# Kernel tuning notes

Measured on AMD Instinct MI355X. Metric: run time of the kernel, lower is better.

The kernel has to match this reference:

```python
import jax, jax.numpy as jnp
import numpy as np

D_MODEL = 64
N_HEADS = 4
HEAD_DIM = D_MODEL // N_HEADS
D_FF = 128
EPS = 1e-5


def _layernorm(x, gamma, beta):
    mu = jnp.mean(x, axis=-1, keepdims=True)
    var = jnp.mean(jnp.square(x - mu), axis=-1, keepdims=True)
    return (x - mu) * jax.lax.rsqrt(var + EPS) * gamma + beta


def setup_inputs() -> dict:
    key = jax.random.key(0)
    ks = jax.random.split(key, 8)
    b, t = 16, 2048
    s = 0.05  # weight init scale
    return {
        "x": jax.random.normal(ks[0], (b, t, D_MODEL), dtype=jnp.float32),
        "Wqkv": jax.random.normal(ks[1], (3 * D_MODEL, D_MODEL), dtype=jnp.float32) * s,
        "Wproj": jax.random.normal(ks[2], (D_MODEL, D_MODEL), dtype=jnp.float32) * s,
        "W1": jax.random.normal(ks[3], (D_FF, D_MODEL), dtype=jnp.float32) * s,
        "b1": jax.random.normal(ks[4], (D_FF,), dtype=jnp.float32) * s,
        "W2": jax.random.normal(ks[5], (D_MODEL, D_FF), dtype=jnp.float32) * s,
        "b2": jax.random.normal(ks[6], (D_MODEL,), dtype=jnp.float32) * s,
        "g1": jnp.ones((D_MODEL,), dtype=jnp.float32),
        "be1": jnp.zeros((D_MODEL,), dtype=jnp.float32),
        "g2": jnp.ones((D_MODEL,), dtype=jnp.float32),
        "be2": jnp.zeros((D_MODEL,), dtype=jnp.float32),
    }


def reference(x, Wqkv, Wproj, W1, b1, W2, b2, g1, be1, g2, be2):
    b, t, c = x.shape
    # qkv: [b,t,3c] -> [b,t,3,h,hd] -> unbind into q,k,v each [b,h,t,hd]
    qkv = jnp.einsum('btc,ec->bte', x, Wqkv)
    qkv = qkv.reshape(b, t, 3, N_HEADS, HEAD_DIM)
    q = jnp.transpose(qkv[:, :, 0], (0, 2, 1, 3))
    k = jnp.transpose(qkv[:, :, 1], (0, 2, 1, 3))
    v = jnp.transpose(qkv[:, :, 2], (0, 2, 1, 3))
    scale = HEAD_DIM ** -0.5
    attn = jnp.einsum('bhqd,bhkd->bhqk', q, k) * scale  # [b,h,t,t]
    attn = jax.nn.softmax(attn, axis=-1)
    a = jnp.einsum('bhqk,bhkd->bhqd', attn, v)          # [b,h,t,hd]
    a = jnp.transpose(a, (0, 2, 1, 3)).reshape(b, t, c)
    a = jnp.einsum('btc,dc->btd', a, Wproj)
    x = _layernorm(x + a, g1, be1)
    y = jnp.einsum('btc,fc->btf', x, W1) + b1
    y = jnp.einsum('btf,cf->btc', jax.nn.relu(y), W2) + b2
    return _layernorm(x + y, g2, be2)
```

## Files before the change

kernel.cpp:

```cpp
#include <hip/hip_runtime.h>
#include <hip/hip_bf16.h>
#include <math.h>

typedef _Float16 h16;
typedef h16   v4h __attribute__((ext_vector_type(4)));
typedef h16   h2  __attribute__((ext_vector_type(2)));
typedef float v4f __attribute__((ext_vector_type(4)));

#define T_SEQ 2048
#define BATCH 16
#define NTOK  (BATCH * T_SEQ)
#define C_DIM 64
#define N_H   4
#define HD    16
#define FF    128
#define EPS_LN 1e-5f
#define MFMA16 __builtin_amdgcn_mfma_f32_16x16x16f16
#define QSCALE (0.25f * 1.44269504089f * 1024.0f)
#define BMAGIC (12582912.0f + 15316.0f)

static __device__ __forceinline__ float frcp(float x) {
#if __has_builtin(__builtin_amdgcn_rcpf)
    return __builtin_amdgcn_rcpf(x);
#else
    return 1.0f / x;
#endif
}
static __device__ __forceinline__ float frsq(float x) {
#if __has_builtin(__builtin_amdgcn_rsqf)
    return __builtin_amdgcn_rsqf(x);
#else
    return rsqrtf(x);
#endif
}
static __device__ __forceinline__ float fdot2p(h2 a, float acc) {
#if __has_builtin(__builtin_amdgcn_fdot2)
    const h2 one2 = {(h16)1.0f, (h16)1.0f};
    return __builtin_amdgcn_fdot2(a, one2, acc, false);
#else
    return acc + (float)a[0] + (float)a[1];
#endif
}
static __device__ __forceinline__ v4h cvt4(v4f f) {
    v4h r; r[0]=(h16)f[0]; r[1]=(h16)f[1]; r[2]=(h16)f[2]; r[3]=(h16)f[3];
    return r;
}
static __device__ __forceinline__ h2 pkperm(float t0, float t1) {
    unsigned r = __builtin_amdgcn_perm(__builtin_bit_cast(unsigned, t1),
                                       __builtin_bit_cast(unsigned, t0),
                                       0x05040100u);
    return __builtin_bit_cast(h2, r);
}

__global__ __launch_bounds__(256) void prep_pack(
    const float* __restrict__ Wqkv, const float* __restrict__ Wproj,
    const float* __restrict__ W1,   const float* __restrict__ W2,
    v4h* __restrict__ wp)
{
    int fid = blockIdx.x * 256 + threadIdx.x;
    int lane = fid & 63;
    int lm = lane & 15, g4 = ((lane >> 4) & 3) * 4;
    int frag = fid >> 6;
    const float* src; int o, kt, K;
    if (fid < 3072)      { int f = frag;      o = f >> 2; kt = f & 3; K = 64;  src = Wqkv;  }
    else if (fid < 4096) { int f = frag - 48; o = f >> 2; kt = f & 3; K = 64;  src = Wproj; }
    else if (fid < 6144) { int f = frag - 64; o = f >> 2; kt = f & 3; K = 64;  src = W1;    }
    else                 { int f = frag - 96; o = f >> 3; kt = f & 7; K = 128; src = W2;    }
    v4f v = *(const v4f*)(src + (o*16 + lm)*K + kt*16 + g4);
    wp[fid] = cvt4(v);
}

__global__ __launch_bounds__(256) void qkv_gemm(
    const float* __restrict__ x, const v4h* __restrict__ wq,
    h16* __restrict__ q, h16* __restrict__ k, h16* __restrict__ vt)
{
    int tid = threadIdx.x;
    int lane = tid & 63, w = tid >> 6;
    int lm = lane & 15, g4 = (lane >> 4) * 4;
    int gw = blockIdx.x * 4 + w;
    int tile = gw >> 2, ng = gw & 3;
    int t0 = tile * 16;

    v4h af[4];
#pragma unroll
    for (int kt = 0; kt < 4; kt++)
        af[kt] = cvt4(*(const v4f*)(x + (size_t)(t0 + lm) * C_DIM + kt * 16 + g4));

    int b = t0 >> 11, tl = t0 & (T_SEQ - 1);
#pragma unroll
    for (int j = 0; j < 3; j++) {
        int n = ng * 3 + j;
        v4f acc = {0.f, 0.f, 0.f, 0.f};
#pragma unroll
        for (int kt = 0; kt < 4; kt++)
            acc = MFMA16(af[kt], wq[(n*4 + kt)*64 + lane], acc, 0, 0, 0);
        if (n < 4) {
            h16* qp = q + ((size_t)(b*N_H + n)*T_SEQ + tl + g4)*HD + lm;
#pragma unroll
            for (int r = 0; r < 4; r++) qp[r*HD] = (h16)(acc[r] * QSCALE);
        } else if (n < 8) {
            h16* kp = k + ((size_t)(b*N_H + (n-4))*T_SEQ + tl + g4)*HD + lm;
#pragma unroll
            for (int r = 0; r < 4; r++) kp[r*HD] = (h16)acc[r];
        } else {
            v4h pk;
#pragma unroll
            for (int r = 0; r < 4; r++) pk[r] = (h16)acc[r];
            *(v4h*)(vt + ((size_t)(b*N_H + (n-8))*(T_SEQ/16) + (tl >> 4))*256
                       + lm*16 + g4) = pk;
        }
    }
}

__global__ __launch_bounds__(256, 8) void attn_mfma(
    const h16* __restrict__ q, const h16* __restrict__ k,
    const h16* __restrict__ vt, h16* __restrict__ a)
{
    int tid = threadIdx.x;
    int lane = tid & 63, w = tid >> 6;
    int lm = lane & 15, g4 = (lane >> 4) * 4;
    int bid = blockIdx.x;
    int W = (bid & 7) * 256 + (bid >> 3);
    int bh = W >> 5;
    int q64 = W & 31;
    int q0 = q64 * 64 + (w & 1) * 32;
    int khalf = w >> 1;

    v4h qf0 = *(const v4h*)(q + ((size_t)bh*T_SEQ + q0      + lm)*HD + g4);
    v4h qf1 = *(const v4h*)(q + ((size_t)bh*T_SEQ + q0 + 16 + lm)*HD + g4);
    const h16* kpl = k  + ((size_t)bh*T_SEQ + khalf*1024 + lm)*HD + g4;
    const h16* vpl = vt + ((size_t)bh*(T_SEQ/16) + khalf*64)*256 + lm*16 + g4;

    v4f accA0={0,0,0,0}, accB0={0,0,0,0}, accA1={0,0,0,0}, accB1={0,0,0,0};
    float l0a = 0.f, l0b = 0.f, l1a = 0.f, l1b = 0.f;
    const v4f bvec = {BMAGIC, BMAGIC, BMAGIC, BMAGIC};

    for (int kt = 0; kt < 16; kt++) {
        v4h kf[4], vf[4];
#pragma unroll
        for (int m = 0; m < 4; m++) {
            kf[m] = *(const v4h*)(kpl + m*256);
            vf[m] = *(const v4h*)(vpl + m*256);
        }
        kpl += 1024; vpl += 1024;
        __builtin_amdgcn_sched_barrier(0);
#pragma unroll
        for (int m = 0; m < 4; m++) {
            v4f t0v = MFMA16(kf[m], qf0, bvec, 0, 0, 0);
            v4f t1v = MFMA16(kf[m], qf1, bvec, 0, 0, 0);
            h2 a0 = pkperm(t0v[0], t0v[1]);
            h2 b0 = pkperm(t0v[2], t0v[3]);
            h2 a1 = pkperm(t1v[0], t1v[1]);
            h2 b1 = pkperm(t1v[2], t1v[3]);
            l0a = fdot2p(a0, l0a); l0b = fdot2p(b0, l0b);
            l1a = fdot2p(a1, l1a); l1b = fdot2p(b1, l1b);
            v4h p0 = __builtin_shufflevector(a0, b0, 0, 1, 2, 3);
            v4h p1 = __builtin_shufflevector(a1, b1, 0, 1, 2, 3);
            if (m & 1) { accB0 = MFMA16(vf[m], p0, accB0, 0,0,0); accB1 = MFMA16(vf[m], p1, accB1, 0,0,0); }
            else       { accA0 = MFMA16(vf[m], p0, accA0, 0,0,0); accA1 = MFMA16(vf[m], p1, accA1, 0,0,0); }
        }
    }

    float l0 = l0a + l0b, l1 = l1a + l1b;
    l0 += __shfl_xor(l0, 16, 64); l0 += __shfl_xor(l0, 32, 64);
    l1 += __shfl_xor(l1, 16, 64); l1 += __shfl_xor(l1, 32, 64);
    v4f acc0 = accA0 + accB0, acc1 = accA1 + accB1;

    __shared__ float lds[2][64][13];
    if (w >= 2) {
        float* p = lds[w - 2][lane];
        p[0] = l0; p[1] = l1;
#pragma unroll
        for (int r = 0; r < 4; r++) { p[2 + r] = acc0[r]; p[6 + r] = acc1[r]; }
    }
    __syncthreads();
    if (w < 2) {
        const float* p = lds[w][lane];
        float inv0 = frcp(l0 + p[0]);
        float inv1 = frcp(l1 + p[1]);
        int b = bh >> 2, h = bh & 3;
        v4h o0, o1;
#pragma unroll
        for (int r = 0; r < 4; r++) {
            o0[r] = (h16)((acc0[r] + p[2 + r]) * inv0);
            o1[r] = (h16)((acc1[r] + p[6 + r]) * inv1);
        }
        *(v4h*)(a + ((size_t)(b*T_SEQ) + q0      + lm)*C_DIM + h*HD + g4) = o0;
        *(v4h*)(a + ((size_t)(b*T_SEQ) + q0 + 16 + lm)*C_DIM + h*HD + g4) = o1;
    }
}

__global__ __launch_bounds__(256) void tail_fused(
    const h16* __restrict__ a, const float* __restrict__ x,
    const v4h* __restrict__ wp,
    const float* __restrict__ b1, const float* __restrict__ b2,
    const float* __restrict__ g1, const float* __restrict__ be1,
    const float* __restrict__ g2, const float* __restrict__ be2,
    float* __restrict__ out)
{
    int tid = threadIdx.x;
    int lane = tid & 63, w = tid >> 6;
    int lm = lane & 15, g4 = (lane >> 4) * 4;
    int pair = w >> 1;
    int half = w & 1;
    int t0 = (blockIdx.x * 2 + pair) * 16;

    const v4h* whp = wp + 3072;
    const v4h* wh1 = wp + 4096;
    const v4h* wh2 = wp + 6144;

    v4h af[4];
#pragma unroll
    for (int kt = 0; kt < 4; kt++)
        af[kt] = *(const v4h*)(a + (size_t)(t0 + lm)*C_DIM + kt*16 + g4);

    float rvn[4][4];
    v4h x1t[4];
    {
        v4h wf[16];
#pragma unroll
        for (int f = 0; f < 16; f++) wf[f] = whp[f*64 + lane];
        __builtin_amdgcn_sched_barrier(0);
        v4f rv[4];
#pragma unroll
        for (int cn = 0; cn < 4; cn++) {
            v4f acc = {0.f, 0.f, 0.f, 0.f};
#pragma unroll
            for (int kt = 0; kt < 4; kt++)
                acc = MFMA16(wf[cn*4 + kt], af[kt], acc, 0, 0, 0);
            v4f xr = *(const v4f*)(x + (size_t)(t0 + lm)*C_DIM + cn*16 + g4);
            rv[cn] = acc + xr;
        }
        float s = 0.f;
#pragma unroll
        for (int cn = 0; cn < 4; cn++)
#pragma unroll
            for (int i = 0; i < 4; i++) s += rv[cn][i];
        s += __shfl_xor(s, 16, 64); s += __shfl_xor(s, 32, 64);
        float mu = s * (1.f/64.f);
        float qs = 0.f;
#pragma unroll
        for (int cn = 0; cn < 4; cn++)
#pragma unroll
            for (int i = 0; i < 4; i++) { float d = rv[cn][i] - mu; qs += d*d; }
        qs += __shfl_xor(qs, 16, 64); qs += __shfl_xor(qs, 32, 64);
        float is = frsq(qs * (1.f/64.f) + EPS_LN);
#pragma unroll
        for (int cn = 0; cn < 4; cn++) {
            v4f g1v = *(const v4f*)(g1 + cn*16 + g4);
            v4f bev = *(const v4f*)(be1 + cn*16 + g4);
#pragma unroll
            for (int i = 0; i < 4; i++) {
                float vl = (rv[cn][i] - mu) * is * g1v[i] + bev[i];
                rvn[cn][i] = vl;
                x1t[cn][i] = (h16)vl;
            }
        }
    }
    __builtin_amdgcn_sched_barrier(0);

    v4h ht[4];
    {
        v4h wf[16];
#pragma unroll
        for (int f = 0; f < 16; f++) wf[f] = wh1[(half*16 + f)*64 + lane];
        __builtin_amdgcn_sched_barrier(0);
#pragma unroll
        for (int j = 0; j < 4; j++) {
            int nf = half * 4 + j;
            v4f acc = {0.f, 0.f, 0.f, 0.f};
#pragma unroll
            for (int kt = 0; kt < 4; kt++)
                acc = MFMA16(wf[j*4 + kt], x1t[kt], acc, 0, 0, 0);
            v4f b1v = *(const v4f*)(b1 + nf*16 + g4);
#pragma unroll
            for (int i = 0; i < 4; i++) ht[j][i] = (h16)fmaxf(acc[i] + b1v[i], 0.f);
        }
    }
    __builtin_amdgcn_sched_barrier(0);

    float yp[4][4];
    {
        v4h wf[16];
#pragma unroll
        for (int cn = 0; cn < 4; cn++)
#pragma unroll
            for (int j = 0; j < 4; j++)
                wf[cn*4 + j] = wh2[(cn*8 + half*4 + j)*64 + lane];
        __builtin_amdgcn_sched_barrier(0);
#pragma unroll
        for (int cn = 0; cn < 4; cn++) {
            v4f acc = {0.f, 0.f, 0.f, 0.f};
#pragma unroll
            for (int j = 0; j < 4; j++)
                acc = MFMA16(wf[cn*4 + j], ht[j], acc, 0, 0, 0);
#pragma unroll
            for (int i = 0; i < 4; i++) yp[cn][i] = acc[i];
        }
    }

    __shared__ float lds[2][64][17];
    if (half == 1) {
        float* p = lds[pair][lane];
#pragma unroll
        for (int cn = 0; cn < 4; cn++)
#pragma unroll
            for (int i = 0; i < 4; i++) p[cn*4 + i] = yp[cn][i];
    }
    __syncthreads();
    if (half == 0) {
        const float* p = lds[pair][lane];
        float yv[4][4];
#pragma unroll
        for (int cn = 0; cn < 4; cn++) {
            v4f b2v = *(const v4f*)(b2 + cn*16 + g4);
#pragma unroll
            for (int i = 0; i < 4; i++)
                yv[cn][i] = yp[cn][i] + p[cn*4 + i] + b2v[i] + rvn[cn][i];
        }
        float s2 = 0.f;
#pragma unroll
        for (int cn = 0; cn < 4; cn++)
#pragma unroll
            for (int i = 0; i < 4; i++) s2 += yv[cn][i];
        s2 += __shfl_xor(s2, 16, 64); s2 += __shfl_xor(s2, 32, 64);
        float mu2 = s2 * (1.f/64.f);
        float qs2 = 0.f;
#pragma unroll
        for (int cn = 0; cn < 4; cn++)
#pragma unroll
            for (int i = 0; i < 4; i++) { float d = yv[cn][i] - mu2; qs2 += d*d; }
        qs2 += __shfl_xor(qs2, 16, 64); qs2 += __shfl_xor(qs2, 32, 64);
        float is2 = frsq(qs2 * (1.f/64.f) + EPS_LN);
#pragma unroll
        for (int cn = 0; cn < 4; cn++) {
            v4f g2v = *(const v4f*)(g2 + cn*16 + g4);
            v4f bev = *(const v4f*)(be2 + cn*16 + g4);
            v4f o;
#pragma unroll
            for (int i = 0; i < 4; i++) o[i] = (yv[cn][i] - mu2) * is2 * g2v[i] + bev[i];
            *(v4f*)(out + (size_t)(t0 + lm)*C_DIM + cn*16 + g4) = o;
        }
    }
}

extern "C" void kernel_launch(void* const* d_in, const int* in_sizes, int n_in,
                              void* d_out, int out_size, void* d_ws, size_t ws_size,
                              hipStream_t stream)
{
    const float* x     = (const float*)d_in[0];
    const float* Wqkv  = (const float*)d_in[1];
    const float* Wproj = (const float*)d_in[2];
    const float* W1    = (const float*)d_in[3];
    const float* b1    = (const float*)d_in[4];
    const float* W2    = (const float*)d_in[5];
    const float* b2    = (const float*)d_in[6];
    const float* g1    = (const float*)d_in[7];
    const float* be1   = (const float*)d_in[8];
    const float* g2    = (const float*)d_in[9];
    const float* be2   = (const float*)d_in[10];
    float* out = (float*)d_out;

    const size_t perQ = (size_t)BATCH * N_H * T_SEQ * HD;
    h16* q   = (h16*)d_ws;
    h16* kk  = q  + perQ;
    h16* vt  = kk + perQ;
    h16* a   = vt + perQ;
    v4h* wp  = (v4h*)(a + (size_t)NTOK * C_DIM);

    prep_pack  <<<32,   256, 0, stream>>>(Wqkv, Wproj, W1, W2, wp);
    qkv_gemm   <<<2048, 256, 0, stream>>>(x, wp, q, kk, vt);
    attn_mfma  <<<2048, 256, 0, stream>>>(q, kk, vt, a);
    tail_fused <<<1024, 256, 0, stream>>>(a, x, wp, b1, b2,
                                          g1, be1, g2, be2, out);
}
```

Baseline: 69.99 us.

## Switch to 16x16x32 f16 MFMA with repacked weights and V layout

Replaces pairs of 16x16x16 MFMAs with the K=32 variant available on MI355X (gfx950) across the QKV GEMM, attention PV product, and tail GEMMs. It repacks the weight fragments and the transposed V buffer into 8-half fragments so each lane loads one 16-byte vector per MFMA. The goal is to halve the MFMA issue count and widen the loads. The PV accumulation now waits for all four score tiles before issuing, which reduces interleaving between the softmax work and the MFMAs.

```diff
diff --git a/kernel.cpp b/kernel.cpp
--- a/kernel.cpp
+++ b/kernel.cpp
@@ -4,6 +4,7 @@
 
 typedef _Float16 h16;
 typedef h16   v4h __attribute__((ext_vector_type(4)));
+typedef h16   v8h __attribute__((ext_vector_type(8)));
 typedef h16   h2  __attribute__((ext_vector_type(2)));
 typedef float v4f __attribute__((ext_vector_type(4)));
 
@@ -16,6 +17,7 @@
 #define FF    128
 #define EPS_LN 1e-5f
 #define MFMA16 __builtin_amdgcn_mfma_f32_16x16x16f16
+#define MFMA32K __builtin_amdgcn_mfma_f32_16x16x32_f16
 #define QSCALE (0.25f * 1.44269504089f * 1024.0f)
 #define BMAGIC (12582912.0f + 15316.0f)
 
@@ -45,6 +47,9 @@
     v4h r; r[0]=(h16)f[0]; r[1]=(h16)f[1]; r[2]=(h16)f[2]; r[3]=(h16)f[3];
     return r;
 }
+static __device__ __forceinline__ v8h cat8(v4h a, v4h b) {
+    return __builtin_shufflevector(a, b, 0, 1, 2, 3, 4, 5, 6, 7);
+}
 static __device__ __forceinline__ h2 pkperm(float t0, float t1) {
     unsigned r = __builtin_amdgcn_perm(__builtin_bit_cast(unsigned, t1),
                                        __builtin_bit_cast(unsigned, t0),
@@ -55,23 +60,28 @@
 __global__ __launch_bounds__(256) void prep_pack(
     const float* __restrict__ Wqkv, const float* __restrict__ Wproj,
     const float* __restrict__ W1,   const float* __restrict__ W2,
-    v4h* __restrict__ wp)
+    v8h* __restrict__ wp)
 {
     int fid = blockIdx.x * 256 + threadIdx.x;
     int lane = fid & 63;
     int lm = lane & 15, g4 = ((lane >> 4) & 3) * 4;
     int frag = fid >> 6;
-    const float* src; int o, kt, K;
-    if (fid < 3072)      { int f = frag;      o = f >> 2; kt = f & 3; K = 64;  src = Wqkv;  }
-    else if (fid < 4096) { int f = frag - 48; o = f >> 2; kt = f & 3; K = 64;  src = Wproj; }
-    else if (fid < 6144) { int f = frag - 64; o = f >> 2; kt = f & 3; K = 64;  src = W1;    }
-    else                 { int f = frag - 96; o = f >> 3; kt = f & 7; K = 128; src = W2;    }
-    v4f v = *(const v4f*)(src + (o*16 + lm)*K + kt*16 + g4);
-    wp[fid] = cvt4(v);
+    const float* src; int o, u, K;
+    if (frag < 24)      { o = frag >> 1;        u = frag & 1; K = 64;  src = Wqkv;  }
+    else if (frag < 32) { o = (frag - 24) >> 1; u = frag & 1; K = 64;  src = Wproj; }
+    else if (frag < 48) { o = (frag - 32) >> 1; u = frag & 1; K = 64;  src = W1;    }
+    else                { o = (frag - 48) >> 2; u = frag & 3; K = 128; src = W2;    }
+    const float* row = src + (size_t)(o*16 + lm) * K + u*32;
+    v4f lo = *(const v4f*)(row + g4);
+    v4f hi = *(const v4f*)(row + 16 + g4);
+    v8h o8;
+#pragma unroll
+    for (int i = 0; i < 4; i++) { o8[i] = (h16)lo[i]; o8[4+i] = (h16)hi[i]; }
+    wp[fid] = o8;
 }
 
 __global__ __launch_bounds__(256) void qkv_gemm(
-    const float* __restrict__ x, const v4h* __restrict__ wq,
+    const float* __restrict__ x, const v8h* __restrict__ wq,
     h16* __restrict__ q, h16* __restrict__ k, h16* __restrict__ vt)
 {
     int tid = threadIdx.x;
@@ -85,15 +95,17 @@
 #pragma unroll
     for (int kt = 0; kt < 4; kt++)
         af[kt] = cvt4(*(const v4f*)(x + (size_t)(t0 + lm) * C_DIM + kt * 16 + g4));
+    v8h a8[2];
+    a8[0] = cat8(af[0], af[1]);
+    a8[1] = cat8(af[2], af[3]);
 
     int b = t0 >> 11, tl = t0 & (T_SEQ - 1);
 #pragma unroll
     for (int j = 0; j < 3; j++) {
         int n = ng * 3 + j;
         v4f acc = {0.f, 0.f, 0.f, 0.f};
-#pragma unroll
-        for (int kt = 0; kt < 4; kt++)
-            acc = MFMA16(af[kt], wq[(n*4 + kt)*64 + lane], acc, 0, 0, 0);
+        acc = MFMA32K(a8[0], wq[(n*2 + 0)*64 + lane], acc, 0, 0, 0);
+        acc = MFMA32K(a8[1], wq[(n*2 + 1)*64 + lane], acc, 0, 0, 0);
         if (n < 4) {
             h16* qp = q + ((size_t)(b*N_H + n)*T_SEQ + tl + g4)*HD + lm;
 #pragma unroll
@@ -106,8 +118,9 @@
             v4h pk;
 #pragma unroll
             for (int r = 0; r < 4; r++) pk[r] = (h16)acc[r];
-            *(v4h*)(vt + ((size_t)(b*N_H + (n-8))*(T_SEQ/16) + (tl >> 4))*256
-                       + lm*16 + g4) = pk;
+            int hv = (tl >> 4) & 1;
+            *(v4h*)(vt + ((size_t)(b*N_H + (n-8))*(T_SEQ/32) + (tl >> 5))*512
+                       + lm*32 + (lane >> 4)*8 + hv*4) = pk;
         }
     }
 }
@@ -129,21 +142,24 @@
     v4h qf0 = *(const v4h*)(q + ((size_t)bh*T_SEQ + q0      + lm)*HD + g4);
     v4h qf1 = *(const v4h*)(q + ((size_t)bh*T_SEQ + q0 + 16 + lm)*HD + g4);
     const h16* kpl = k  + ((size_t)bh*T_SEQ + khalf*1024 + lm)*HD + g4;
-    const h16* vpl = vt + ((size_t)bh*(T_SEQ/16) + khalf*64)*256 + lm*16 + g4;
+    const h16* vpl = vt + ((size_t)bh*(T_SEQ/32) + khalf*32)*512
+                        + lm*32 + (lane >> 4)*8;
 
     v4f accA0={0,0,0,0}, accB0={0,0,0,0}, accA1={0,0,0,0}, accB1={0,0,0,0};
     float l0a = 0.f, l0b = 0.f, l1a = 0.f, l1b = 0.f;
     const v4f bvec = {BMAGIC, BMAGIC, BMAGIC, BMAGIC};
 
     for (int kt = 0; kt < 16; kt++) {
-        v4h kf[4], vf[4];
-#pragma unroll
-        for (int m = 0; m < 4; m++) {
+        v4h kf[4];
+        v8h vf8[2];
+#pragma unroll
+        for (int m = 0; m < 4; m++)
             kf[m] = *(const v4h*)(kpl + m*256);
-            vf[m] = *(const v4h*)(vpl + m*256);
-        }
+        vf8[0] = *(const v8h*)(vpl);
+        vf8[1] = *(const v8h*)(vpl + 512);
         kpl += 1024; vpl += 1024;
         __builtin_amdgcn_sched_barrier(0);
+        v4h p0[4], p1[4];
 #pragma unroll
         for (int m = 0; m < 4; m++) {
             v4f t0v = MFMA16(kf[m], qf0, bvec, 0, 0, 0);
@@ -154,11 +170,13 @@
             h2 b1 = pkperm(t1v[2], t1v[3]);
             l0a = fdot2p(a0, l0a); l0b = fdot2p(b0, l0b);
             l1a = fdot2p(a1, l1a); l1b = fdot2p(b1, l1b);
-            v4h p0 = __builtin_shufflevector(a0, b0, 0, 1, 2, 3);
-            v4h p1 = __builtin_shufflevector(a1, b1, 0, 1, 2, 3);
-            if (m & 1) { accB0 = MFMA16(vf[m], p0, accB0, 0,0,0); accB1 = MFMA16(vf[m], p1, accB1, 0,0,0); }
-            else       { accA0 = MFMA16(vf[m], p0, accA0, 0,0,0); accA1 = MFMA16(vf[m], p1, accA1, 0,0,0); }
-        }
+            p0[m] = __builtin_shufflevector(a0, b0, 0, 1, 2, 3);
+            p1[m] = __builtin_shufflevector(a1, b1, 0, 1, 2, 3);
+        }
+        accA0 = MFMA32K(vf8[0], cat8(p0[0], p0[1]), accA0, 0, 0, 0);
+        accA1 = MFMA32K(vf8[0], cat8(p1[0], p1[1]), accA1, 0, 0, 0);
+        accB0 = MFMA32K(vf8[1], cat8(p0[2], p0[3]), accB0, 0, 0, 0);
+        accB1 = MFMA32K(vf8[1], cat8(p1[2], p1[3]), accB1, 0, 0, 0);
     }
 
     float l0 = l0a + l0b, l1 = l1a + l1b;
@@ -192,7 +210,7 @@
 
 __global__ __launch_bounds__(256) void tail_fused(
     const h16* __restrict__ a, const float* __restrict__ x,
-    const v4h* __restrict__ wp,
+    const v8h* __restrict__ wp,
     const float* __restrict__ b1, const float* __restrict__ b2,
     const float* __restrict__ g1, const float* __restrict__ be1,
     const float* __restrict__ g2, const float* __restrict__ be2,
@@ -205,29 +223,31 @@
     int half = w & 1;
     int t0 = (blockIdx.x * 2 + pair) * 16;
 
-    const v4h* whp = wp + 3072;
-    const v4h* wh1 = wp + 4096;
-    const v4h* wh2 = wp + 6144;
+    const v8h* whp = wp + 24*64;
+    const v8h* wh1 = wp + 32*64;
+    const v8h* wh2 = wp + 48*64;
 
     v4h af[4];
 #pragma unroll
     for (int kt = 0; kt < 4; kt++)
         af[kt] = *(const v4h*)(a + (size_t)(t0 + lm)*C_DIM + kt*16 + g4);
+    v8h a8[2];
+    a8[0] = cat8(af[0], af[1]);
+    a8[1] = cat8(af[2], af[3]);
 
     float rvn[4][4];
-    v4h x1t[4];
+    v8h x8[2];
     {
-        v4h wf[16];
-#pragma unroll
-        for (int f = 0; f < 16; f++) wf[f] = whp[f*64 + lane];
+        v8h wf[8];
+#pragma unroll
+        for (int f = 0; f < 8; f++) wf[f] = whp[f*64 + lane];
         __builtin_amdgcn_sched_barrier(0);
         v4f rv[4];
 #pragma unroll
         for (int cn = 0; cn < 4; cn++) {
             v4f acc = {0.f, 0.f, 0.f, 0.f};
-#pragma unroll
-            for (int kt = 0; kt < 4; kt++)
-                acc = MFMA16(wf[cn*4 + kt], af[kt], acc, 0, 0, 0);
+            acc = MFMA32K(wf[cn*2 + 0], a8[0], acc, 0, 0, 0);
+            acc = MFMA32K(wf[cn*2 + 1], a8[1], acc, 0, 0, 0);
             v4f xr = *(const v4f*)(x + (size_t)(t0 + lm)*C_DIM + cn*16 + g4);
             rv[cn] = acc + xr;
         }
@@ -245,6 +265,7 @@
             for (int i = 0; i < 4; i++) { float d = rv[cn][i] - mu; qs += d*d; }
         qs += __shfl_xor(qs, 16, 64); qs += __shfl_xor(qs, 32, 64);
         float is = frsq(qs * (1.f/64.f) + EPS_LN);
+        v4h x1t[4];
 #pragma unroll
         for (int cn = 0; cn < 4; cn++) {
             v4f g1v = *(const v4f*)(g1 + cn*16 + g4);
@@ -256,44 +277,51 @@
                 x1t[cn][i] = (h16)vl;
             }
         }
+        x8[0] = cat8(x1t[0], x1t[1]);
+        x8[1] = cat8(x1t[2], x1t[3]);
     }
     __builtin_amdgcn_sched_barrier(0);
 
-    v4h ht[4];
+    v8h h8[2];
     {
-        v4h wf[16];
-#pragma unroll
-        for (int f = 0; f < 16; f++) wf[f] = wh1[(half*16 + f)*64 + lane];
+        v8h wf[8];
+#pragma unroll
+        for (int j = 0; j < 4; j++) {
+            int nf = half * 4 + j;
+            wf[j*2]     = wh1[(nf*2 + 0)*64 + lane];
+            wf[j*2 + 1] = wh1[(nf*2 + 1)*64 + lane];
+        }
         __builtin_amdgcn_sched_barrier(0);
+        v4h ht[4];
 #pragma unroll
         for (int j = 0; j < 4; j++) {
             int nf = half * 4 + j;
             v4f acc = {0.f, 0.f, 0.f, 0.f};
-#pragma unroll
-            for (int kt = 0; kt < 4; kt++)
-                acc = MFMA16(wf[j*4 + kt], x1t[kt], acc, 0, 0, 0);
+            acc = MFMA32K(wf[j*2],     x8[0], acc, 0, 0, 0);
+            acc = MFMA32K(wf[j*2 + 1], x8[1], acc, 0, 0, 0);
             v4f b1v = *(const v4f*)(b1 + nf*16 + g4);
 #pragma unroll
             for (int i = 0; i < 4; i++) ht[j][i] = (h16)fmaxf(acc[i] + b1v[i], 0.f);
         }
+        h8[0] = cat8(ht[0], ht[1]);
+        h8[1] = cat8(ht[2], ht[3]);
     }
     __builtin_amdgcn_sched_barrier(0);
 
     float yp[4][4];
     {
-        v4h wf[16];
-#pragma unroll
-        for (int cn = 0; cn < 4; cn++)
-#pragma unroll
-            for (int j = 0; j < 4; j++)
-                wf[cn*4 + j] = wh2[(cn*8 + half*4 + j)*64 + lane];
+        v8h wf[8];
+#pragma unroll
+        for (int cn = 0; cn < 4; cn++)
+#pragma unroll
+            for (int v = 0; v < 2; v++)
+                wf[cn*2 + v] = wh2[(cn*4 + 2*half + v)*64 + lane];
         __builtin_amdgcn_sched_barrier(0);
 #pragma unroll
         for (int cn = 0; cn < 4; cn++) {
             v4f acc = {0.f, 0.f, 0.f, 0.f};
-#pragma unroll
-            for (int j = 0; j < 4; j++)
-                acc = MFMA16(wf[cn*4 + j], ht[j], acc, 0, 0, 0);
+            acc = MFMA32K(wf[cn*2],     h8[0], acc, 0, 0, 0);
+            acc = MFMA32K(wf[cn*2 + 1], h8[1], acc, 0, 0, 0);
 #pragma unroll
             for (int i = 0; i < 4; i++) yp[cn][i] = acc[i];
         }
@@ -366,9 +394,9 @@
     h16* kk  = q  + perQ;
     h16* vt  = kk + perQ;
     h16* a   = vt + perQ;
-    v4h* wp  = (v4h*)(a + (size_t)NTOK * C_DIM);
-
-    prep_pack  <<<32,   256, 0, stream>>>(Wqkv, Wproj, W1, W2, wp);
+    v8h* wp  = (v8h*)(a + (size_t)NTOK * C_DIM);
+
+    prep_pack  <<<16,   256, 0, stream>>>(Wqkv, Wproj, W1, W2, wp);
     qkv_gemm   <<<2048, 256, 0, stream>>>(x, wp, q, kk, vt);
     attn_mfma  <<<2048, 256, 0, stream>>>(q, kk, vt, a);
     tail_fused <<<1024, 256, 0, stream>>>(a, x, wp, b1, b2,
```

After: 75.19 us. 7.4% more time.

## Prefetch K tiles one step ahead in attention and share x tile via LDS

Applied to the files above, without the earlier changes.

The attention loop now double-buffers K fragments in registers, loading the next K block while computing the current one, and lowers the occupancy hint from 8 to 6 to allow more registers. The QKV GEMM now assigns one block per 16-token tile and stages x once in shared memory, converted to half precision, instead of having each wave reload and convert it. This is meant to hide global load latency in attention and reduce redundant x loads. In exchange, register pressure and possibly occupancy change, and the last iteration prefetches K past the end of the per-head range.

```diff
diff --git a/kernel.cpp b/kernel.cpp
--- a/kernel.cpp
+++ b/kernel.cpp
@@ -77,14 +77,23 @@
     int tid = threadIdx.x;
     int lane = tid & 63, w = tid >> 6;
     int lm = lane & 15, g4 = (lane >> 4) * 4;
-    int gw = blockIdx.x * 4 + w;
-    int tile = gw >> 2, ng = gw & 3;
+    int tile = blockIdx.x;
     int t0 = tile * 16;
+    int ng = w;
+
+    __shared__ h16 xs[16][72];
+    {
+        v4f v = *(const v4f*)(x + (size_t)t0 * C_DIM + tid * 4);
+        int r = tid >> 4;
+        int c = (tid & 15) * 4;
+        *(v4h*)&xs[r][c] = cvt4(v);
+    }
+    __syncthreads();
 
     v4h af[4];
 #pragma unroll
     for (int kt = 0; kt < 4; kt++)
-        af[kt] = cvt4(*(const v4f*)(x + (size_t)(t0 + lm) * C_DIM + kt * 16 + g4));
+        af[kt] = *(const v4h*)&xs[lm][kt*16 + g4];
 
     int b = t0 >> 11, tl = t0 & (T_SEQ - 1);
 #pragma unroll
@@ -112,7 +121,7 @@
     }
 }
 
-__global__ __launch_bounds__(256, 8) void attn_mfma(
+__global__ __launch_bounds__(256, 6) void attn_mfma(
     const h16* __restrict__ q, const h16* __restrict__ k,
     const h16* __restrict__ vt, h16* __restrict__ a)
 {
@@ -135,31 +144,45 @@
     float l0a = 0.f, l0b = 0.f, l1a = 0.f, l1b = 0.f;
     const v4f bvec = {BMAGIC, BMAGIC, BMAGIC, BMAGIC};
 
-    for (int kt = 0; kt < 16; kt++) {
-        v4h kf[4], vf[4];
-#pragma unroll
-        for (int m = 0; m < 4; m++) {
-            kf[m] = *(const v4h*)(kpl + m*256);
-            vf[m] = *(const v4h*)(vpl + m*256);
-        }
-        kpl += 1024; vpl += 1024;
-        __builtin_amdgcn_sched_barrier(0);
-#pragma unroll
-        for (int m = 0; m < 4; m++) {
-            v4f t0v = MFMA16(kf[m], qf0, bvec, 0, 0, 0);
-            v4f t1v = MFMA16(kf[m], qf1, bvec, 0, 0, 0);
-            h2 a0 = pkperm(t0v[0], t0v[1]);
-            h2 b0 = pkperm(t0v[2], t0v[3]);
-            h2 a1 = pkperm(t1v[0], t1v[1]);
-            h2 b1 = pkperm(t1v[2], t1v[3]);
-            l0a = fdot2p(a0, l0a); l0b = fdot2p(b0, l0b);
-            l1a = fdot2p(a1, l1a); l1b = fdot2p(b1, l1b);
-            v4h p0 = __builtin_shufflevector(a0, b0, 0, 1, 2, 3);
-            v4h p1 = __builtin_shufflevector(a1, b1, 0, 1, 2, 3);
-            if (m & 1) { accB0 = MFMA16(vf[m], p0, accB0, 0,0,0); accB1 = MFMA16(vf[m], p1, accB1, 0,0,0); }
-            else       { accA0 = MFMA16(vf[m], p0, accA0, 0,0,0); accA1 = MFMA16(vf[m], p1, accA1, 0,0,0); }
-        }
-    }
+    v4h kfA[4], kfB[4];
+#pragma unroll
+    for (int m = 0; m < 4; m++) kfA[m] = *(const v4h*)(kpl + m*256);
+    kpl += 1024;
+
+#define ATTN_BODY(KCUR, KNXT)                                                 \
+    {                                                                         \
+        v4h vf[4];                                                            \
+        _Pragma("unroll")                                                     \
+        for (int m = 0; m < 4; m++) vf[m] = *(const v4h*)(vpl + m*256);       \
+        _Pragma("unroll")                                                     \
+        for (int m = 0; m < 4; m++) KNXT[m] = *(const v4h*)(kpl + m*256);     \
+        vpl += 1024; kpl += 1024;                                             \
+        __builtin_amdgcn_sched_barrier(0);                                    \
+        _Pragma("unroll")                                                     \
+        for (int m = 0; m < 4; m++) {                                         \
+            v4f t0v = MFMA16(KCUR[m], qf0, bvec, 0, 0, 0);                    \
+            v4f t1v = MFMA16(KCUR[m], qf1, bvec, 0, 0, 0);                    \
+            h2 a0 = pkperm(t0v[0], t0v[1]);                                   \
+            h2 b0 = pkperm(t0v[2], t0v[3]);                                   \
+            h2 a1 = pkperm(t1v[0], t1v[1]);                                   \
+            h2 b1 = pkperm(t1v[2], t1v[3]);                                   \
+            l0a = fdot2p(a0, l0a); l0b = fdot2p(b0, l0b);                     \
+            l1a = fdot2p(a1, l1a); l1b = fdot2p(b1, l1b);                     \
+            v4h p0 = __builtin_shufflevector(a0, b0, 0, 1, 2, 3);             \
+            v4h p1 = __builtin_shufflevector(a1, b1, 0, 1, 2, 3);             \
+            if (m & 1) { accB0 = MFMA16(vf[m], p0, accB0, 0,0,0);             \
+                         accB1 = MFMA16(vf[m], p1, accB1, 0,0,0); }           \
+            else       { accA0 = MFMA16(vf[m], p0, accA0, 0,0,0);             \
+                         accA1 = MFMA16(vf[m], p1, accA1, 0,0,0); }           \
+        }                                                                     \
+        __builtin_amdgcn_sched_barrier(0);                                    \
+    }
+
+    for (int kt = 0; kt < 16; kt += 2) {
+        ATTN_BODY(kfA, kfB)
+        ATTN_BODY(kfB, kfA)
+    }
+#undef ATTN_BODY
 
     float l0 = l0a + l0b, l1 = l1a + l1b;
     l0 += __shfl_xor(l0, 16, 64); l0 += __shfl_xor(l0, 32, 64);
```

Result: no change. 69.00 us (-1.4%).

## Widen attention query tile per wave and stage x tile in LDS for QKV

Applied to the files above, without the earlier changes.

The attention kernel now processes four 16-row query fragments per wave (128 queries per block) instead of two, so each loaded K/V fragment is reused across twice as many queries. Grid size halves and the occupancy hint drops from 8 to 4 blocks per CU to make room for the larger accumulator register footprint. Separately, the QKV GEMM now loads each 16-token x tile once into shared memory per block and has all four waves read it from there, instead of each wave re-reading and converting from global memory. The trade-off is higher register pressure and fewer resident waves in attention, plus an extra barrier in the GEMM.

```diff
diff --git a/kernel.cpp b/kernel.cpp
--- a/kernel.cpp
+++ b/kernel.cpp
@@ -77,14 +77,23 @@
     int tid = threadIdx.x;
     int lane = tid & 63, w = tid >> 6;
     int lm = lane & 15, g4 = (lane >> 4) * 4;
-    int gw = blockIdx.x * 4 + w;
-    int tile = gw >> 2, ng = gw & 3;
+    int tile = blockIdx.x;
     int t0 = tile * 16;
+    int ng = w;
+
+    __shared__ h16 xs[16][72];
+    {
+        v4f v = *(const v4f*)(x + (size_t)t0 * C_DIM + tid * 4);
+        int r = tid >> 4;
+        int c = (tid & 15) * 4;
+        *(v4h*)&xs[r][c] = cvt4(v);
+    }
+    __syncthreads();
 
     v4h af[4];
 #pragma unroll
     for (int kt = 0; kt < 4; kt++)
-        af[kt] = cvt4(*(const v4f*)(x + (size_t)(t0 + lm) * C_DIM + kt * 16 + g4));
+        af[kt] = *(const v4h*)&xs[lm][kt*16 + g4];
 
     int b = t0 >> 11, tl = t0 & (T_SEQ - 1);
 #pragma unroll
@@ -112,7 +121,7 @@
     }
 }
 
-__global__ __launch_bounds__(256, 8) void attn_mfma(
+__global__ __launch_bounds__(256, 4) void attn_mfma(
     const h16* __restrict__ q, const h16* __restrict__ k,
     const h16* __restrict__ vt, h16* __restrict__ a)
 {
@@ -120,19 +129,22 @@
     int lane = tid & 63, w = tid >> 6;
     int lm = lane & 15, g4 = (lane >> 4) * 4;
     int bid = blockIdx.x;
-    int W = (bid & 7) * 256 + (bid >> 3);
-    int bh = W >> 5;
-    int q64 = W & 31;
-    int q0 = q64 * 64 + (w & 1) * 32;
+    int W = (bid & 7) * 128 + (bid >> 3);
+    int bh = W >> 4;
+    int q128 = W & 15;
+    int q0 = q128 * 128 + (w & 1) * 64;
     int khalf = w >> 1;
 
-    v4h qf0 = *(const v4h*)(q + ((size_t)bh*T_SEQ + q0      + lm)*HD + g4);
-    v4h qf1 = *(const v4h*)(q + ((size_t)bh*T_SEQ + q0 + 16 + lm)*HD + g4);
+    v4h qf[4];
+#pragma unroll
+    for (int j = 0; j < 4; j++)
+        qf[j] = *(const v4h*)(q + ((size_t)bh*T_SEQ + q0 + j*16 + lm)*HD + g4);
     const h16* kpl = k  + ((size_t)bh*T_SEQ + khalf*1024 + lm)*HD + g4;
     const h16* vpl = vt + ((size_t)bh*(T_SEQ/16) + khalf*64)*256 + lm*16 + g4;
 
-    v4f accA0={0,0,0,0}, accB0={0,0,0,0}, accA1={0,0,0,0}, accB1={0,0,0,0};
-    float l0a = 0.f, l0b = 0.f, l1a = 0.f, l1b = 0.f;
+    v4f accA[4] = {{0,0,0,0},{0,0,0,0},{0,0,0,0},{0,0,0,0}};
+    v4f accB[4] = {{0,0,0,0},{0,0,0,0},{0,0,0,0},{0,0,0,0}};
+    float la[4] = {0.f,0.f,0.f,0.f}, lb[4] = {0.f,0.f,0.f,0.f};
     const v4f bvec = {BMAGIC, BMAGIC, BMAGIC, BMAGIC};
 
     for (int kt = 0; kt < 16; kt++) {
@@ -146,47 +158,53 @@
         __builtin_amdgcn_sched_barrier(0);
 #pragma unroll
         for (int m = 0; m < 4; m++) {
-            v4f t0v = MFMA16(kf[m], qf0, bvec, 0, 0, 0);
-            v4f t1v = MFMA16(kf[m], qf1, bvec, 0, 0, 0);
-            h2 a0 = pkperm(t0v[0], t0v[1]);
-            h2 b0 = pkperm(t0v[2], t0v[3]);
-            h2 a1 = pkperm(t1v[0], t1v[1]);
-            h2 b1 = pkperm(t1v[2], t1v[3]);
-            l0a = fdot2p(a0, l0a); l0b = fdot2p(b0, l0b);
-            l1a = fdot2p(a1, l1a); l1b = fdot2p(b1, l1b);
-            v4h p0 = __builtin_shufflevector(a0, b0, 0, 1, 2, 3);
-            v4h p1 = __builtin_shufflevector(a1, b1, 0, 1, 2, 3);
-            if (m & 1) { accB0 = MFMA16(vf[m], p0, accB0, 0,0,0); accB1 = MFMA16(vf[m], p1, accB1, 0,0,0); }
-            else       { accA0 = MFMA16(vf[m], p0, accA0, 0,0,0); accA1 = MFMA16(vf[m], p1, accA1, 0,0,0); }
-        }
-    }
-
-    float l0 = l0a + l0b, l1 = l1a + l1b;
-    l0 += __shfl_xor(l0, 16, 64); l0 += __shfl_xor(l0, 32, 64);
-    l1 += __shfl_xor(l1, 16, 64); l1 += __shfl_xor(l1, 32, 64);
-    v4f acc0 = accA0 + accB0, acc1 = accA1 + accB1;
-
-    __shared__ float lds[2][64][13];
+#pragma unroll
+            for (int j = 0; j < 4; j++) {
+                v4f t = MFMA16(kf[m], qf[j], bvec, 0, 0, 0);
+                h2 a0 = pkperm(t[0], t[1]);
+                h2 b0 = pkperm(t[2], t[3]);
+                la[j] = fdot2p(a0, la[j]);
+                lb[j] = fdot2p(b0, lb[j]);
+                v4h p = __builtin_shufflevector(a0, b0, 0, 1, 2, 3);
+                if (m & 1) accB[j] = MFMA16(vf[m], p, accB[j], 0, 0, 0);
+                else       accA[j] = MFMA16(vf[m], p, accA[j], 0, 0, 0);
+            }
+        }
+    }
+
+    float l[4];
+    v4f acc[4];
+#pragma unroll
+    for (int j = 0; j < 4; j++) {
+        float lj = la[j] + lb[j];
+        lj += __shfl_xor(lj, 16, 64); lj += __shfl_xor(lj, 32, 64);
+        l[j] = lj;
+        acc[j] = accA[j] + accB[j];
+    }
+
+    __shared__ float lds[2][64][21];
     if (w >= 2) {
         float* p = lds[w - 2][lane];
-        p[0] = l0; p[1] = l1;
-#pragma unroll
-        for (int r = 0; r < 4; r++) { p[2 + r] = acc0[r]; p[6 + r] = acc1[r]; }
+#pragma unroll
+        for (int j = 0; j < 4; j++) {
+            p[j] = l[j];
+#pragma unroll
+            for (int r = 0; r < 4; r++) p[4 + j*4 + r] = acc[j][r];
+        }
     }
     __syncthreads();
     if (w < 2) {
         const float* p = lds[w][lane];
-        float inv0 = frcp(l0 + p[0]);
-        float inv1 = frcp(l1 + p[1]);
         int b = bh >> 2, h = bh & 3;
-        v4h o0, o1;
-#pragma unroll
-        for (int r = 0; r < 4; r++) {
-            o0[r] = (h16)((acc0[r] + p[2 + r]) * inv0);
-            o1[r] = (h16)((acc1[r] + p[6 + r]) * inv1);
-        }
-        *(v4h*)(a + ((size_t)(b*T_SEQ) + q0      + lm)*C_DIM + h*HD + g4) = o0;
-        *(v4h*)(a + ((size_t)(b*T_SEQ) + q0 + 16 + lm)*C_DIM + h*HD + g4) = o1;
+#pragma unroll
+        for (int j = 0; j < 4; j++) {
+            float inv = frcp(l[j] + p[j]);
+            v4h o;
+#pragma unroll
+            for (int r = 0; r < 4; r++)
+                o[r] = (h16)((acc[j][r] + p[4 + j*4 + r]) * inv);
+            *(v4h*)(a + ((size_t)(b*T_SEQ) + q0 + j*16 + lm)*C_DIM + h*HD + g4) = o;
+        }
     }
 }
 
@@ -370,7 +388,7 @@
 
     prep_pack  <<<32,   256, 0, stream>>>(Wqkv, Wproj, W1, W2, wp);
     qkv_gemm   <<<2048, 256, 0, stream>>>(x, wp, q, kk, vt);
-    attn_mfma  <<<2048, 256, 0, stream>>>(q, kk, vt, a);
+    attn_mfma  <<<1024, 256, 0, stream>>>(q, kk, vt, a);
     tail_fused <<<1024, 256, 0, stream>>>(a, x, wp, b1, b2,
                                           g1, be1, g2, be2, out);
 }
```

New measurement: 63.77 us. -8.9%, faster.
